# Kernel tuning notes

Measured on AMD Instinct MI355X. Metric: run time of the kernel, lower is better.

The kernel has to match this reference:

```python
import jax, jax.numpy as jnp
import numpy as np

HIDDEN = 1024
HEADS = 16
HEAD_DIM = HIDDEN // HEADS


def setup_inputs() -> dict:
    key = jax.random.key(0)
    k_x, k_wa, k_ba, k_wp, k_bp = jax.random.split(key, 5)
    x = jax.random.normal(k_x, (2, 2048, HIDDEN), dtype=jnp.float32)
    s_a = 1.0 / np.sqrt(HIDDEN)
    # torch Linear default init ~ U(-1/sqrt(fan_in), 1/sqrt(fan_in)); stored as [in, out]
    W_attn = jax.random.uniform(k_wa, (HIDDEN, 3 * HIDDEN), jnp.float32, -s_a, s_a)
    b_attn = jax.random.uniform(k_ba, (3 * HIDDEN,), jnp.float32, -s_a, s_a)
    W_proj = jax.random.uniform(k_wp, (HIDDEN, HIDDEN), jnp.float32, -s_a, s_a)
    b_proj = jax.random.uniform(k_bp, (HIDDEN,), jnp.float32, -s_a, s_a)
    return {"x": x, "W_attn": W_attn, "b_attn": b_attn, "W_proj": W_proj, "b_proj": b_proj}


def reference(x, W_attn, b_attn, W_proj, b_proj):
    B, S, D = x.shape
    H, Hd = HEADS, HEAD_DIM
    qkv = x @ W_attn + b_attn                     # [B, S, 3D]
    q, k, v = jnp.split(qkv, 3, axis=-1)
    # [B, H, S, Hd]
    q = q.reshape(B, S, H, Hd).transpose(0, 2, 1, 3)
    k = k.reshape(B, S, H, Hd).transpose(0, 2, 1, 3)
    v = v.reshape(B, S, H, Hd).transpose(0, 2, 1, 3)
    scale = 1.0 / np.sqrt(Hd).astype(np.float32)
    scores = jnp.einsum('bhqd,bhkd->bhqk', q, k) * scale   # [B, H, S, S]
    causal = jnp.triu(jnp.ones((S, S), dtype=bool), k=1)   # True above diagonal
    scores = jnp.where(causal, -jnp.inf, scores)
    probs = jax.nn.softmax(scores, axis=-1)
    # dropout p=0.0 -> identity (eval-mode equivalent)
    ctx = jnp.einsum('bhqk,bhkd->bhqd', probs, v)           # [B, H, S, Hd]
    ctx = ctx.transpose(0, 2, 1, 3).reshape(B, S, D)
    return ctx @ W_proj + b_proj
```

## Files before the change

### kernel.cpp

```cpp
#include <hip/hip_runtime.h>
#include <hip/hip_bf16.h>
#include <stdint.h>

#define HID 1024
#define NH 16
#define HD 64
#define SEQ 2048
#define BATCH 2
#define M_TOT 4096
#define QSCALE 0.18033688011112042f

typedef __attribute__((ext_vector_type(8))) short short8;
typedef __attribute__((ext_vector_type(4))) float f32x4;
typedef __hip_bfloat16 bf16;

__device__ __forceinline__ void load_lds16(const void* g, void* l) {
  __builtin_amdgcn_global_load_lds(
      (const __attribute__((address_space(1))) unsigned int*)g,
      (__attribute__((address_space(3))) unsigned int*)l, 16, 0, 0);
}

__device__ __forceinline__ unsigned short f2bf_bits(float f) {
  __hip_bfloat16 h = __float2bfloat16(f);
  return *reinterpret_cast<unsigned short*>(&h);
}
__device__ __forceinline__ unsigned pack2bf(float a, float b) {
  return (unsigned)f2bf_bits(a) | ((unsigned)f2bf_bits(b) << 16);
}
__device__ __forceinline__ unsigned cvt_pk_bf16(float a, float b) {
  unsigned r;
  asm("v_cvt_pk_bf16_f32 %0, %1, %2" : "=v"(r) : "v"(a), "v"(b));
  return r;
}

__global__ void cvt_f32_to_bf16(const float* __restrict__ in,
                                bf16* __restrict__ out, int n4) {
  int i = blockIdx.x * blockDim.x + threadIdx.x;
  if (i >= n4) return;
  float4 v = reinterpret_cast<const float4*>(in)[i];
  ushort4 o;
  o.x = f2bf_bits(v.x); o.y = f2bf_bits(v.y);
  o.z = f2bf_bits(v.z); o.w = f2bf_bits(v.w);
  reinterpret_cast<ushort4*>(out)[i] = o;
}

__global__ void transpose_cvt2(const float* __restrict__ Wa, bf16* __restrict__ WTa,
                               const float* __restrict__ Wp, bf16* __restrict__ WTp) {
  __shared__ float tile[32][33];
  int bx = blockIdx.x;
  const float* W; bf16* WT; int N;
  if (bx < 96) { W = Wa; WT = WTa; N = 3072; }
  else         { W = Wp; WT = WTp; N = 1024; bx -= 96; }
  const int K = 1024;
  int n0 = bx * 32, k0 = blockIdx.y * 32;
  int tx = threadIdx.x, ty = threadIdx.y;
#pragma unroll
  for (int i = 0; i < 32; i += 8)
    tile[ty + i][tx] = W[(size_t)(k0 + ty + i) * N + n0 + tx];
  __syncthreads();
#pragma unroll
  for (int i = 0; i < 32; i += 8)
    WT[(size_t)(n0 + ty + i) * K + k0 + tx] = __float2bfloat16(tile[tx][ty + i]);
}

template <int EPI>
__global__ __launch_bounds__(256, 2)
void gemm128(const bf16* __restrict__ A, const bf16* __restrict__ BT,
             const float* __restrict__ bias,
             bf16* __restrict__ Qo, bf16* __restrict__ Ko, bf16* __restrict__ Vo,
             float* __restrict__ Fo) {
  const int Kdim = 1024;
  __shared__ bf16 As[128 * 64];
  __shared__ bf16 Bs[128 * 64];
  const int tid = threadIdx.x;
  const int wid = tid >> 6, lane = tid & 63;
  const int m0 = blockIdx.x * 128;
  const int n0 = blockIdx.y * 128;
  const int wrow = (wid >> 1) * 64, wcol = (wid & 1) * 64;

  f32x4 acc[4][4];
#pragma unroll
  for (int rb = 0; rb < 4; ++rb)
#pragma unroll
    for (int cb = 0; cb < 4; ++cb)
      acc[rb][cb] = (f32x4){0.f, 0.f, 0.f, 0.f};

  const int lr = lane >> 3;
  const int cc = lane & 7;
  const int lc = cc * 8;
  const int fr = lane & 15, fk = (lane >> 4) * 8;

  for (int kt = 0; kt < Kdim / 64; ++kt) {
    __syncthreads();
#pragma unroll
    for (int t = 0; t < 4; ++t) {
      int i = wid * 4 + t;
      int row = i * 8 + lr;
      load_lds16(A + (size_t)(m0 + row) * Kdim + kt * 64 + lc, (char*)As + i * 1024);
      load_lds16(BT + (size_t)(n0 + row) * Kdim + kt * 64 + lc, (char*)Bs + i * 1024);
    }
    __syncthreads();

    short8 af[4][2], bf_[4][2];
#pragma unroll
    for (int rb = 0; rb < 4; ++rb)
#pragma unroll
      for (int kk = 0; kk < 2; ++kk) {
        af[rb][kk] = *(const short8*)&As[(wrow + rb * 16 + fr) * 64 + kk * 32 + fk];
        bf_[rb][kk] = *(const short8*)&Bs[(wcol + rb * 16 + fr) * 64 + kk * 32 + fk];
      }
#pragma unroll
    for (int rb = 0; rb < 4; ++rb)
#pragma unroll
      for (int cb = 0; cb < 4; ++cb)
#pragma unroll
        for (int kk = 0; kk < 2; ++kk)
          acc[rb][cb] = __builtin_amdgcn_mfma_f32_16x16x32_bf16(
              af[rb][kk], bf_[cb][kk], acc[rb][cb], 0, 0, 0);
  }

  const int fg = (lane >> 4) * 4;
  float bv[4];
#pragma unroll
  for (int cb = 0; cb < 4; ++cb) bv[cb] = bias[n0 + wcol + cb * 16 + fr];

  if (EPI == 0) {
    __syncthreads();
    char* ep = (wid < 2 ? (char*)As : (char*)Bs) + (wid & 1) * 8192;
    const int ncol = n0 + wcol;
    const int part = ncol >> 10;
    const int h = (ncol & 1023) >> 6;
    const int b = m0 >> 11;
    const int s_base = (m0 + wrow) & 2047;
    const size_t hb = (size_t)(b * NH + h);

    if (part < 2) {
      const float qs = (part == 0) ? QSCALE : 1.f;
#pragma unroll
      for (int rb = 0; rb < 4; ++rb)
#pragma unroll
        for (int cb = 0; cb < 4; ++cb)
#pragma unroll
          for (int j = 0; j < 4; ++j) {
            int row = rb * 16 + fg + j;
            int colb = (cb * 16 + fr) * 2;
            *(unsigned short*)(ep + row * 128 + (colb ^ ((row & 7) << 4))) =
                f2bf_bits((acc[rb][cb][j] + bv[cb]) * qs);
          }
      bf16* dst = (part == 0 ? Qo : Ko) + hb * SEQ * HD;
#pragma unroll
      for (int p = 0; p < 8; ++p) {
        int row = p * 8 + lr;
        uint4 v = *(const uint4*)(ep + row * 128 + ((cc * 16) ^ ((row & 7) << 4)));
        *(uint4*)(dst + (size_t)(s_base + row) * HD + cc * 8) = v;
      }
    } else {
#pragma unroll
      for (int rb = 0; rb < 4; ++rb)
#pragma unroll
        for (int cb = 0; cb < 4; ++cb) {
          int cV = cb * 16 + fr;
          int r0 = (rb * 16 + fg) * 2;
          uint2 wv;
          wv.x = pack2bf(acc[rb][cb][0] + bv[cb], acc[rb][cb][1] + bv[cb]);
          wv.y = pack2bf(acc[rb][cb][2] + bv[cb], acc[rb][cb][3] + bv[cb]);
          *(uint2*)(ep + cV * 128 + (r0 ^ ((cV & 7) << 4))) = wv;
        }
      bf16* dstV = Vo + hb * HD * SEQ;
#pragma unroll
      for (int p = 0; p < 8; ++p) {
        int hd = p * 8 + lr;
        uint4 v = *(const uint4*)(ep + hd * 128 + ((cc * 16) ^ ((hd & 7) << 4)));
        *(uint4*)(dstV + (size_t)hd * SEQ + s_base + cc * 8) = v;
      }
    }
  } else {
#pragma unroll
    for (int rb = 0; rb < 4; ++rb) {
      int r0 = m0 + wrow + rb * 16 + fg;
#pragma unroll
      for (int cb = 0; cb < 4; ++cb) {
        int n = n0 + wcol + cb * 16 + fr;
#pragma unroll
        for (int j = 0; j < 4; ++j)
          Fo[(size_t)(r0 + j) * HID + n] = acc[rb][cb][j] + bv[cb];
      }
    }
  }
}

__global__ __launch_bounds__(256, 4)
void attn_kernel(const bf16* __restrict__ Q, const bf16* __restrict__ K,
                 const bf16* __restrict__ VT, bf16* __restrict__ ctx) {
  __shared__ char smem[40960];
  const int tid = threadIdx.x, wid = tid >> 6, lane = tid & 63;
  const int idx = blockIdx.x;
  const int qt = (idx < 512) ? (31 - (idx >> 5)) : ((idx - 512) >> 5);
  const int bh = idx & 31;
  const int b = bh >> 4, h = bh & 15;
  const size_t base = (size_t)bh * SEQ * HD;
  const int q0 = qt * 64 + wid * 16;

  const int fr16 = lane & 15, hi4 = lane >> 4;
  const int lr = lane >> 3;
  const int cc = lane & 7;
  const int qg = q0 + fr16;
  const int gc = (cc ^ lr) * 8;
  const int pswz = (fr16 & 7) << 4;
  char* pp = smem + 32768 + wid * 2048;

  short8 qf[2];
  const bf16* qp = Q + base + (size_t)qg * HD;
#pragma unroll
  for (int kc = 0; kc < 2; ++kc)
    qf[kc] = *(const short8*)(qp + kc * 32 + hi4 * 8);

  f32x4 oa[4], ob[4];
#pragma unroll
  for (int dg = 0; dg < 4; ++dg) {
    oa[dg] = (f32x4){0.f, 0.f, 0.f, 0.f};
    ob[dg] = (f32x4){0.f, 0.f, 0.f, 0.f};
  }
  float lpart = 0.f;

  auto stage_tile = [&](int tt) {
    char* nb = smem + (tt & 1) * 16384;
    const int nv = tt * 64;
#pragma unroll
    for (int t = 0; t < 4; ++t) {
      int c = wid * 4 + t;
      if (c < 8)
        load_lds16(K + base + (size_t)(nv + c * 8 + lr) * HD + gc, nb + c * 1024);
      else
        load_lds16(VT + base + (size_t)((c - 8) * 8 + lr) * SEQ + nv + gc,
                   nb + 8192 + (c - 8) * 1024);
    }
  };

  auto tile_compute = [&](const char* sb, int kv0, f32x4 (&oc)[4]) {
    f32x4 sa[4];
    __builtin_amdgcn_s_setprio(1);
#pragma unroll
    for (int kb = 0; kb < 4; ++kb) {
      sa[kb] = (f32x4){0.f, 0.f, 0.f, 0.f};
      const int row = kb * 16 + fr16;
      const int swz = (row & 7) << 4;
#pragma unroll
      for (int kc = 0; kc < 2; ++kc) {
        short8 kf = *(const short8*)(sb + row * 128 + ((kc * 64 + hi4 * 16) ^ swz));
        sa[kb] = __builtin_amdgcn_mfma_f32_16x16x32_bf16(kf, qf[kc], sa[kb], 0, 0, 0);
      }
    }
    __builtin_amdgcn_s_setprio(0);

    if (kv0 + 63 > q0) {
#pragma unroll
      for (int kb = 0; kb < 4; ++kb)
#pragma unroll
        for (int j = 0; j < 4; ++j) {
          int kvg = kv0 + kb * 16 + hi4 * 4 + j;
          sa[kb][j] = (kvg > qg) ? -1e30f : sa[kb][j];
        }
    }

    float s0 = 0.f, s1 = 0.f, s2 = 0.f, s3 = 0.f;
#pragma unroll
    for (int kb = 0; kb < 4; ++kb) {
      float e0 = __builtin_exp2f(sa[kb][0]);
      float e1 = __builtin_exp2f(sa[kb][1]);
      float e2 = __builtin_exp2f(sa[kb][2]);
      float e3 = __builtin_exp2f(sa[kb][3]);
      sa[kb][0] = e0; sa[kb][1] = e1; sa[kb][2] = e2; sa[kb][3] = e3;
      s0 += e0; s1 += e1; s2 += e2; s3 += e3;
    }
    lpart += (s0 + s1) + (s2 + s3);

#pragma unroll
    for (int kb = 0; kb < 4; ++kb) {
      uint2 u;
      u.x = cvt_pk_bf16(sa[kb][0], sa[kb][1]);
      u.y = cvt_pk_bf16(sa[kb][2], sa[kb][3]);
      *(uint2*)(pp + fr16 * 128 + ((kb * 32 + hi4 * 8) ^ pswz)) = u;
    }
    short8 pfrag[2];
#pragma unroll
    for (int ks = 0; ks < 2; ++ks)
      pfrag[ks] = *(const short8*)(pp + fr16 * 128 + ((ks * 64 + hi4 * 16) ^ pswz));

    const char* sv = sb + 8192;
    __builtin_amdgcn_s_setprio(1);
#pragma unroll
    for (int dg = 0; dg < 4; ++dg) {
      const int row = dg * 16 + fr16;
#pragma unroll
      for (int ks = 0; ks < 2; ++ks) {
        short8 vf = *(const short8*)(sv + row * 128 + ((ks * 64 + hi4 * 16) ^ pswz));
        oc[dg] = __builtin_amdgcn_mfma_f32_16x16x32_bf16(vf, pfrag[ks], oc[dg], 0, 0, 0);
      }
    }
    __builtin_amdgcn_s_setprio(0);
  };

  const int ntiles = qt + 1;

  stage_tile(0);

  for (int t = 0; t < ntiles; ++t) {
    const char* sb = smem + (t & 1) * 16384;

    __builtin_amdgcn_s_barrier();
    __builtin_amdgcn_sched_barrier(0);

    if (t + 1 < ntiles) {
      stage_tile(t + 1);
      asm volatile("s_waitcnt vmcnt(4)" ::: "memory");
    } else {
      asm volatile("s_waitcnt vmcnt(0)" ::: "memory");
    }
    __builtin_amdgcn_sched_barrier(0);

    __builtin_amdgcn_s_barrier();
    __builtin_amdgcn_sched_barrier(0);

    const int kv0 = t * 64;
    if (kv0 <= q0 + 15) {
      if (t & 1) tile_compute(sb, kv0, ob);
      else       tile_compute(sb, kv0, oa);
    }
  }

  float lrun = lpart + __shfl_xor(lpart, 16);
  lrun += __shfl_xor(lrun, 32);
  const float inv = 1.f / lrun;
#pragma unroll
  for (int dg = 0; dg < 4; ++dg) {
    float v0 = (oa[dg][0] + ob[dg][0]) * inv;
    float v1 = (oa[dg][1] + ob[dg][1]) * inv;
    float v2 = (oa[dg][2] + ob[dg][2]) * inv;
    float v3 = (oa[dg][3] + ob[dg][3]) * inv;
    uint2 wv; wv.x = pack2bf(v0, v1); wv.y = pack2bf(v2, v3);
    *(uint2*)(pp + fr16 * 128 + ((dg * 32 + hi4 * 8) ^ pswz)) = wv;
  }
#pragma unroll
  for (int p = 0; p < 2; ++p) {
    int qr = p * 8 + lr;
    uint4 v = *(const uint4*)(pp + qr * 128 + ((cc * 16) ^ ((qr & 7) << 4)));
    int s = q0 + qr;
    *(uint4*)(ctx + (size_t)(b * SEQ + s) * HID + h * 64 + cc * 8) = v;
  }
}

extern "C" void kernel_launch(void* const* d_in, const int* in_sizes, int n_in,
                              void* d_out, int out_size, void* d_ws, size_t ws_size,
                              hipStream_t stream) {
  const float* x      = (const float*)d_in[0];
  const float* W_attn = (const float*)d_in[1];
  const float* b_attn = (const float*)d_in[2];
  const float* W_proj = (const float*)d_in[3];
  const float* b_proj = (const float*)d_in[4];
  float* out = (float*)d_out;

  char* ws = (char*)d_ws;
  const size_t MB = 1u << 20;
  bf16* xb   = (bf16*)(ws + 0);
  bf16* WTa  = (bf16*)(ws + 8 * MB);
  bf16* WTp  = (bf16*)(ws + 14 * MB);
  bf16* Qw   = (bf16*)(ws + 16 * MB);
  bf16* Kw   = (bf16*)(ws + 24 * MB);
  bf16* VTw  = (bf16*)(ws + 32 * MB);
  bf16* ctxb = (bf16*)(ws + 40 * MB);

  cvt_f32_to_bf16<<<(M_TOT * HID / 4 + 255) / 256, 256, 0, stream>>>(x, xb, M_TOT * HID / 4);
  transpose_cvt2<<<dim3(128, 32), dim3(32, 8), 0, stream>>>(W_attn, WTa, W_proj, WTp);

  gemm128<0><<<dim3(M_TOT / 128, 3 * HID / 128), 256, 0, stream>>>(
      xb, WTa, b_attn, Qw, Kw, VTw, nullptr);

  attn_kernel<<<dim3(1024), 256, 0, stream>>>(Qw, Kw, VTw, ctxb);

  gemm128<1><<<dim3(M_TOT / 128, HID / 128), 256, 0, stream>>>(
      ctxb, WTp, b_proj, nullptr, nullptr, nullptr, out);
}
```

Measured before the change: 115.5 us.

## Fuse prep kernels, double-buffer GEMM LDS, and widen attention blocks to 128 queries

Merges the x conversion and weight transpose into one prep launch to cut a kernel launch. The projection GEMM now double-buffers its LDS tiles with XOR swizzling and raises MFMA priority, so global loads overlap compute instead of being serialized by syncthreads. The attention kernel moves to 512-thread blocks covering 128 queries, staging pairs of 64-key tiles so each K/V load is shared by twice as many waves. The costs are more LDS per block (64KB in the GEMM, 80KB in attention), which can lower occupancy, and coarser causal work imbalance.

```diff
diff --git a/kernel.cpp b/kernel.cpp
--- a/kernel.cpp
+++ b/kernel.cpp
@@ -33,27 +33,27 @@
   return r;
 }
 
-__global__ void cvt_f32_to_bf16(const float* __restrict__ in,
-                                bf16* __restrict__ out, int n4) {
-  int i = blockIdx.x * blockDim.x + threadIdx.x;
-  if (i >= n4) return;
-  float4 v = reinterpret_cast<const float4*>(in)[i];
-  ushort4 o;
-  o.x = f2bf_bits(v.x); o.y = f2bf_bits(v.y);
-  o.z = f2bf_bits(v.z); o.w = f2bf_bits(v.w);
-  reinterpret_cast<ushort4*>(out)[i] = o;
-}
-
-__global__ void transpose_cvt2(const float* __restrict__ Wa, bf16* __restrict__ WTa,
-                               const float* __restrict__ Wp, bf16* __restrict__ WTp) {
+__global__ void prep_all(const float* __restrict__ x, bf16* __restrict__ xb,
+                         const float* __restrict__ Wa, bf16* __restrict__ WTa,
+                         const float* __restrict__ Wp, bf16* __restrict__ WTp) {
   __shared__ float tile[32][33];
   int bx = blockIdx.x;
-  const float* W; bf16* WT; int N;
-  if (bx < 96) { W = Wa; WT = WTa; N = 3072; }
-  else         { W = Wp; WT = WTp; N = 1024; bx -= 96; }
+  if (bx < 4096) {
+    int i = bx * 256 + threadIdx.x;
+    float4 v = reinterpret_cast<const float4*>(x)[i];
+    ushort4 o;
+    o.x = f2bf_bits(v.x); o.y = f2bf_bits(v.y);
+    o.z = f2bf_bits(v.z); o.w = f2bf_bits(v.w);
+    reinterpret_cast<ushort4*>(xb)[i] = o;
+    return;
+  }
+  bx -= 4096;
+  const float* W; bf16* WT; int N, tpr;
+  if (bx < 3072) { W = Wa; WT = WTa; N = 3072; tpr = 96; }
+  else           { W = Wp; WT = WTp; N = 1024; tpr = 32; bx -= 3072; }
   const int K = 1024;
-  int n0 = bx * 32, k0 = blockIdx.y * 32;
-  int tx = threadIdx.x, ty = threadIdx.y;
+  int n0 = (bx % tpr) * 32, k0 = (bx / tpr) * 32;
+  int tx = threadIdx.x & 31, ty = threadIdx.x >> 5;
 #pragma unroll
   for (int i = 0; i < 32; i += 8)
     tile[ty + i][tx] = W[(size_t)(k0 + ty + i) * N + n0 + tx];
@@ -70,8 +70,7 @@
              bf16* __restrict__ Qo, bf16* __restrict__ Ko, bf16* __restrict__ Vo,
              float* __restrict__ Fo) {
   const int Kdim = 1024;
-  __shared__ bf16 As[128 * 64];
-  __shared__ bf16 Bs[128 * 64];
+  __shared__ char smem[65536];
   const int tid = threadIdx.x;
   const int wid = tid >> 6, lane = tid & 63;
   const int m0 = blockIdx.x * 128;
@@ -87,28 +86,54 @@
 
   const int lr = lane >> 3;
   const int cc = lane & 7;
-  const int lc = cc * 8;
-  const int fr = lane & 15, fk = (lane >> 4) * 8;
-
-  for (int kt = 0; kt < Kdim / 64; ++kt) {
-    __syncthreads();
+  const int gc = (cc ^ lr) * 8;
+  const int fr = lane & 15;
+  const int fk2 = (lane >> 4) * 16;
+  const int fswz = (fr & 7) << 4;
+
+  auto stage = [&](int kt) {
+    char* nb = smem + (kt & 1) * 32768;
 #pragma unroll
     for (int t = 0; t < 4; ++t) {
       int i = wid * 4 + t;
       int row = i * 8 + lr;
-      load_lds16(A + (size_t)(m0 + row) * Kdim + kt * 64 + lc, (char*)As + i * 1024);
-      load_lds16(BT + (size_t)(n0 + row) * Kdim + kt * 64 + lc, (char*)Bs + i * 1024);
-    }
-    __syncthreads();
+      load_lds16(A + (size_t)(m0 + row) * Kdim + kt * 64 + gc, nb + i * 1024);
+      load_lds16(BT + (size_t)(n0 + row) * Kdim + kt * 64 + gc,
+                 nb + 16384 + i * 1024);
+    }
+  };
+
+  stage(0);
+
+  for (int kt = 0; kt < Kdim / 64; ++kt) {
+    const char* Asc = smem + (kt & 1) * 32768;
+    const char* Bsc = Asc + 16384;
+
+    __builtin_amdgcn_s_barrier();
+    __builtin_amdgcn_sched_barrier(0);
+
+    if (kt + 1 < Kdim / 64) {
+      stage(kt + 1);
+      asm volatile("s_waitcnt vmcnt(8)" ::: "memory");
+    } else {
+      asm volatile("s_waitcnt vmcnt(0)" ::: "memory");
+    }
+    __builtin_amdgcn_sched_barrier(0);
+
+    __builtin_amdgcn_s_barrier();
+    __builtin_amdgcn_sched_barrier(0);
 
     short8 af[4][2], bf_[4][2];
 #pragma unroll
     for (int rb = 0; rb < 4; ++rb)
 #pragma unroll
       for (int kk = 0; kk < 2; ++kk) {
-        af[rb][kk] = *(const short8*)&As[(wrow + rb * 16 + fr) * 64 + kk * 32 + fk];
-        bf_[rb][kk] = *(const short8*)&Bs[(wcol + rb * 16 + fr) * 64 + kk * 32 + fk];
-      }
+        af[rb][kk] = *(const short8*)(Asc + (wrow + rb * 16 + fr) * 128 +
+                                      ((kk * 64 + fk2) ^ fswz));
+        bf_[rb][kk] = *(const short8*)(Bsc + (wcol + rb * 16 + fr) * 128 +
+                                       ((kk * 64 + fk2) ^ fswz));
+      }
+    __builtin_amdgcn_s_setprio(1);
 #pragma unroll
     for (int rb = 0; rb < 4; ++rb)
 #pragma unroll
@@ -117,6 +142,7 @@
         for (int kk = 0; kk < 2; ++kk)
           acc[rb][cb] = __builtin_amdgcn_mfma_f32_16x16x32_bf16(
               af[rb][kk], bf_[cb][kk], acc[rb][cb], 0, 0, 0);
+    __builtin_amdgcn_s_setprio(0);
   }
 
   const int fg = (lane >> 4) * 4;
@@ -126,7 +152,7 @@
 
   if (EPI == 0) {
     __syncthreads();
-    char* ep = (wid < 2 ? (char*)As : (char*)Bs) + (wid & 1) * 8192;
+    char* ep = smem + wid * 8192;
     const int ncol = n0 + wcol;
     const int part = ncol >> 10;
     const int h = (ncol & 1023) >> 6;
@@ -189,17 +215,17 @@
   }
 }
 
-__global__ __launch_bounds__(256, 4)
+__global__ __launch_bounds__(512, 4)
 void attn_kernel(const bf16* __restrict__ Q, const bf16* __restrict__ K,
                  const bf16* __restrict__ VT, bf16* __restrict__ ctx) {
-  __shared__ char smem[40960];
+  __shared__ char smem[81920];
   const int tid = threadIdx.x, wid = tid >> 6, lane = tid & 63;
   const int idx = blockIdx.x;
-  const int qt = (idx < 512) ? (31 - (idx >> 5)) : ((idx - 512) >> 5);
+  const int qt = (idx < 256) ? (15 - (idx >> 5)) : ((idx - 256) >> 5);
   const int bh = idx & 31;
   const int b = bh >> 4, h = bh & 15;
   const size_t base = (size_t)bh * SEQ * HD;
-  const int q0 = qt * 64 + wid * 16;
+  const int q0 = qt * 128 + wid * 16;
 
   const int fr16 = lane & 15, hi4 = lane >> 4;
   const int lr = lane >> 3;
@@ -207,7 +233,7 @@
   const int qg = q0 + fr16;
   const int gc = (cc ^ lr) * 8;
   const int pswz = (fr16 & 7) << 4;
-  char* pp = smem + 32768 + wid * 2048;
+  char* pp = smem + 65536 + wid * 2048;
 
   short8 qf[2];
   const bf16* qp = Q + base + (size_t)qg * HD;
@@ -223,17 +249,19 @@
   }
   float lpart = 0.f;
 
-  auto stage_tile = [&](int tt) {
-    char* nb = smem + (tt & 1) * 16384;
-    const int nv = tt * 64;
+  auto stage_pair = [&](int jp) {
+    char* nb = smem + (jp & 1) * 32768;
+    const int nv = jp * 128;
 #pragma unroll
     for (int t = 0; t < 4; ++t) {
       int c = wid * 4 + t;
-      if (c < 8)
-        load_lds16(K + base + (size_t)(nv + c * 8 + lr) * HD + gc, nb + c * 1024);
-      else
-        load_lds16(VT + base + (size_t)((c - 8) * 8 + lr) * SEQ + nv + gc,
-                   nb + 8192 + (c - 8) * 1024);
+      int reg = c >> 3, crow = (c & 7) * 8 + lr;
+      const bf16* src;
+      if (reg == 0)      src = K + base + (size_t)(nv + crow) * HD + gc;
+      else if (reg == 1) src = VT + base + (size_t)crow * SEQ + nv + gc;
+      else if (reg == 2) src = K + base + (size_t)(nv + 64 + crow) * HD + gc;
+      else               src = VT + base + (size_t)crow * SEQ + nv + 64 + gc;
+      load_lds16(src, nb + c * 1024);
     }
   };
 
@@ -301,18 +329,18 @@
     __builtin_amdgcn_s_setprio(0);
   };
 
-  const int ntiles = qt + 1;
-
-  stage_tile(0);
-
-  for (int t = 0; t < ntiles; ++t) {
-    const char* sb = smem + (t & 1) * 16384;
+  const int npair = qt + 1;
+
+  stage_pair(0);
+
+  for (int j = 0; j < npair; ++j) {
+    char* sb = smem + (j & 1) * 32768;
 
     __builtin_amdgcn_s_barrier();
     __builtin_amdgcn_sched_barrier(0);
 
-    if (t + 1 < ntiles) {
-      stage_tile(t + 1);
+    if (j + 1 < npair) {
+      stage_pair(j + 1);
       asm volatile("s_waitcnt vmcnt(4)" ::: "memory");
     } else {
       asm volatile("s_waitcnt vmcnt(0)" ::: "memory");
@@ -322,11 +350,9 @@
     __builtin_amdgcn_s_barrier();
     __builtin_amdgcn_sched_barrier(0);
 
-    const int kv0 = t * 64;
-    if (kv0 <= q0 + 15) {
-      if (t & 1) tile_compute(sb, kv0, ob);
-      else       tile_compute(sb, kv0, oa);
-    }
+    const int kv0 = j * 128;
+    if (kv0 <= q0 + 15)      tile_compute(sb,         kv0,      oa);
+    if (kv0 + 64 <= q0 + 15) tile_compute(sb + 16384, kv0 + 64, ob);
   }
 
   float lrun = lpart + __shfl_xor(lpart, 16);
@@ -370,13 +396,12 @@
   bf16* VTw  = (bf16*)(ws + 32 * MB);
   bf16* ctxb = (bf16*)(ws + 40 * MB);
 
-  cvt_f32_to_bf16<<<(M_TOT * HID / 4 + 255) / 256, 256, 0, stream>>>(x, xb, M_TOT * HID / 4);
-  transpose_cvt2<<<dim3(128, 32), dim3(32, 8), 0, stream>>>(W_attn, WTa, W_proj, WTp);
+  prep_all<<<dim3(8192), 256, 0, stream>>>(x, xb, W_attn, WTa, W_proj, WTp);
 
   gemm128<0><<<dim3(M_TOT / 128, 3 * HID / 128), 256, 0, stream>>>(
       xb, WTa, b_attn, Qw, Kw, VTw, nullptr);
 
-  attn_kernel<<<dim3(1024), 256, 0, stream>>>(Qw, Kw, VTw, ctxb);
+  attn_kernel<<<dim3(512), 512, 0, stream>>>(Qw, Kw, VTw, ctxb);
 
   gemm128<1><<<dim3(M_TOT / 128, HID / 128), 256, 0, stream>>>(
       ctxb, WTp, b_proj, nullptr, nullptr, nullptr, out);
```

New measurement: 100.9 us. 1.14x faster.
